# Kernel tuning notes

Measured on AMD Instinct MI355X. Metric: run time of the kernel, lower is better.

The kernel has to match this reference:

```python
import jax, jax.numpy as jnp
import numpy as np

H = 300          # node_hidden_dim (GINE output dim)
D = 2 * H        # set2set in_channels = 600
STEPS = 2        # num_step_set2_set


def _lstm_cell(x, h, c, W_ih, W_hh, b_ih, b_hh):
    # PyTorch LSTM gate order: i, f, g, o
    gates = x @ W_ih.T + h @ W_hh.T + b_ih + b_hh
    i, f, g, o = jnp.split(gates, 4, axis=-1)
    c = jax.nn.sigmoid(f) * c + jax.nn.sigmoid(i) * jnp.tanh(g)
    h = jax.nn.sigmoid(o) * jnp.tanh(c)
    return h, c


def _set2set(x, batch, num_graphs, W_ih, W_hh, b_ih, b_hh):
    # torch_geometric Set2Set with processing_steps=STEPS, 1-layer LSTM
    B = num_graphs
    q_star = jnp.zeros((B, 2 * D), x.dtype)
    h = jnp.zeros((B, D), x.dtype)
    c = jnp.zeros((B, D), x.dtype)
    for _ in range(STEPS):
        h, c = _lstm_cell(q_star, h, c, W_ih, W_hh, b_ih, b_hh)
        q = h                                   # [B, D]
        e = jnp.sum(x * q[batch], axis=-1)      # [N]
        emax = jax.ops.segment_max(e, batch, num_segments=B)
        a = jnp.exp(e - emax[batch])
        asum = jax.ops.segment_sum(a, batch, num_segments=B)
        a = a / (asum[batch] + 1e-16)           # segment softmax
        r = jax.ops.segment_sum(a[:, None] * x, batch, num_segments=B)
        q_star = jnp.concatenate([q, r], axis=-1)   # [B, 2D]
    return q_star


def _l2norm(x):
    return x / jnp.maximum(jnp.linalg.norm(x, axis=1, keepdims=True), 1e-12)


def setup_inputs() -> dict:
    key = jax.random.key(0)
    ks = jax.random.split(key, 8)
    Nu, Nv, B = 8192, 8192, 256
    solute_x = jax.random.normal(ks[0], (Nu, H), jnp.float32)
    solvent_x = jax.random.normal(ks[1], (Nv, H), jnp.float32)
    solute_batch = jnp.sort(jax.random.randint(ks[2], (Nu,), 0, B)).astype(jnp.int32)
    solvent_batch = jnp.sort(jax.random.randint(ks[3], (Nv,), 0, B)).astype(jnp.int32)
    lstm_W_ih = jax.random.normal(ks[4], (4 * D, 2 * D), jnp.float32) * 0.02
    lstm_W_hh = jax.random.normal(ks[5], (4 * D, D), jnp.float32) * 0.02
    lstm_b_ih = jnp.zeros((4 * D,), jnp.float32)
    lstm_b_hh = jnp.zeros((4 * D,), jnp.float32)
    pred_W = jax.random.normal(ks[6], (1, 8 * H), jnp.float32) * 0.02
    pred_b = jnp.zeros((1,), jnp.float32)
    return {
        "solute_x": solute_x, "solvent_x": solvent_x,
        "solute_batch": solute_batch, "solvent_batch": solvent_batch,
        "num_graphs": B,
        "lstm_W_ih": lstm_W_ih, "lstm_W_hh": lstm_W_hh,
        "lstm_b_ih": lstm_b_ih, "lstm_b_hh": lstm_b_hh,
        "pred_W": pred_W, "pred_b": pred_b,
    }


def reference(solute_x, solvent_x, solute_batch, solvent_batch, num_graphs,
              lstm_W_ih, lstm_W_hh, lstm_b_ih, lstm_b_hh, pred_W, pred_b):
    # F.normalize(dim=1)
    su = _l2norm(solute_x)    # [Nu, H]
    sv = _l2norm(solvent_x)   # [Nv, H]
    # len_map = solute_len.T @ solvent_len == same-pair membership mask
    mask = (solute_batch[:, None] == solvent_batch[None, :]).astype(su.dtype)
    interaction_map = (su @ sv.T) * mask          # [Nu, Nv]
    ret_interaction_map = interaction_map
    solvent_prime = interaction_map.T @ su        # [Nv, H]
    solute_prime = interaction_map @ sv           # [Nu, H]
    su2 = jnp.concatenate([su, solute_prime], axis=1)    # [Nu, 2H]
    sv2 = jnp.concatenate([sv, solvent_prime], axis=1)   # [Nv, 2H]
    su_s2s = _set2set(su2, solute_batch, num_graphs, lstm_W_ih, lstm_W_hh, lstm_b_ih, lstm_b_hh)
    sv_s2s = _set2set(sv2, solvent_batch, num_graphs, lstm_W_ih, lstm_W_hh, lstm_b_ih, lstm_b_hh)
    final = jnp.concatenate([su_s2s, sv_s2s], axis=1)    # [B, 8H]
    predictions = final @ pred_W.T + pred_b              # [B, 1]
    return predictions, ret_interaction_map
```

## Files before the change

kernel.cpp:

```cpp
#include <hip/hip_runtime.h>
#include <math.h>

#define HDIM 300
#define DDIM 600
#define NGR  256

typedef float vf4 __attribute__((ext_vector_type(4)));
typedef float vf2 __attribute__((ext_vector_type(2)));

__device__ __forceinline__ float wred_sum(float v){
  #pragma unroll
  for(int o=32;o;o>>=1) v += __shfl_xor(v,o,64);
  return v;
}
__device__ __forceinline__ float wred_max(float v){
  #pragma unroll
  for(int o=32;o;o>>=1) v = fmaxf(v,__shfl_xor(v,o,64));
  return v;
}
__device__ __forceinline__ float sigm(float x){ return 1.f/(1.f+expf(-x)); }

__device__ __forceinline__ void fill_row(int i, const int* __restrict__ ub,
    const int* __restrict__ voff, float* __restrict__ mapbase, int Nv, int tid){
  int g = ub[i];
  int js = voff[g], je = voff[g+1];
  float* mrow = mapbase + (size_t)i*Nv;
  const vf4 z4 = {0.f,0.f,0.f,0.f};
  int nf4 = Nv >> 2;
  for (int q4=tid; q4<nf4; q4+=256){
    int j0 = q4*4;
    if (j0+4 <= js || j0 >= je){
      __builtin_nontemporal_store(z4, (vf4*)(mrow + j0));
    } else {
      #pragma unroll
      for(int u=0;u<4;u++){ int j=j0+u; if (j<js || j>=je) mrow[j]=0.f; }
    }
  }
}

__global__ __launch_bounds__(256) void k_norm_off(const float* __restrict__ xu,
    const float* __restrict__ xv, float* __restrict__ su, float* __restrict__ sv,
    int Nu, int Nv, const int* __restrict__ ub, const int* __restrict__ vb,
    int* __restrict__ uoff, int* __restrict__ voff,
    const float* __restrict__ b_ih, const float* __restrict__ b_hh,
    float* __restrict__ h1, float* __restrict__ c1,
    const float* __restrict__ pb, float* __restrict__ outp,
    const float* __restrict__ Wih, const float* __restrict__ Whh,
    float* __restrict__ gbase){
  int NBn = (Nu + Nv) >> 2;
  int b = blockIdx.x;
  int tid = threadIdx.x, lane = tid & 63, w = tid >> 6;
  if (b == NBn){
    int t = tid;
    if (t < NGR){
      int lo=0, hi=Nu;
      while(lo<hi){ int m=(lo+hi)>>1; if (ub[m] < t) lo=m+1; else hi=m; }
      uoff[t]=lo;
      lo=0; hi=Nv;
      while(lo<hi){ int m=(lo+hi)>>1; if (vb[m] < t) lo=m+1; else hi=m; }
      voff[t]=lo;
      if (t==0){ uoff[NGR]=Nu; voff[NGR]=Nv; }
      outp[t] = pb[0];
    }
    for (int d=tid; d<DDIM; d+=256){
      float gi = b_ih[d]      + b_hh[d];
      float gg = b_ih[1200+d] + b_hh[1200+d];
      float go = b_ih[1800+d] + b_hh[1800+d];
      float c  = sigm(gi)*tanhf(gg);
      c1[d]=c; h1[d]=sigm(go)*tanhf(c);
    }
    return;
  }
  if (b > NBn){
    __shared__ float h1l[DDIM];
    for (int d=tid; d<DDIM; d+=256){
      float gi = b_ih[d]      + b_hh[d];
      float gg = b_ih[1200+d] + b_hh[1200+d];
      float go = b_ih[1800+d] + b_hh[1800+d];
      float c  = sigm(gi)*tanhf(gg);
      h1l[d]   = sigm(go)*tanhf(c);
    }
    __syncthreads();
    int n = (b - NBn - 1)*4 + w;
    const float* wi = Wih + (size_t)n*1200;
    const float* wh = Whh + (size_t)n*600;
    float s = 0.f;
    for (int k=lane; k<DDIM; k+=64) s += h1l[k]*(wi[k] + wh[k]);
    s = wred_sum(s);
    if (lane==0) gbase[n] = s + b_ih[n] + b_hh[n];
    return;
  }
  int wid = b*4 + w;
  const float* src; float* dst;
  if (wid < Nu){ src = xu + (size_t)wid*HDIM; dst = su + (size_t)wid*HDIM; }
  else         { src = xv + (size_t)(wid-Nu)*HDIM; dst = sv + (size_t)(wid-Nu)*HDIM; }
  const vf4* s4 = (const vf4*)src;
  vf4 A = s4[lane];
  vf4 Bv = (lane<11)? s4[64+lane] : (vf4){0.f,0.f,0.f,0.f};
  float s = A.x*A.x+A.y*A.y+A.z*A.z+A.w*A.w + Bv.x*Bv.x+Bv.y*Bv.y+Bv.z*Bv.z+Bv.w*Bv.w;
  s = wred_sum(s);
  float inv = 1.f / fmaxf(sqrtf(s), 1e-12f);
  vf4* d4 = (vf4*)dst;
  d4[lane] = A*inv;
  if (lane<11) d4[64+lane] = Bv*inv;
}

__global__ __launch_bounds__(256) void k_prime(const float* __restrict__ su,
    const float* __restrict__ sv, const int* __restrict__ ub,
    const int* __restrict__ vb, const int* __restrict__ uoff,
    const int* __restrict__ voff, float* __restrict__ spr,
    float* __restrict__ svp, float* __restrict__ e1u, float* __restrict__ e1v,
    const float* __restrict__ h1, float* __restrict__ mapbase, int Nu, int Nv){
  int b = blockIdx.x;
  int tid = threadIdx.x, lane = tid & 63, w = tid >> 6;
  int r = b % 3;
  if (r == 2){ fill_row(b/3, ub, voff, mapbase, Nv, tid); return; }
  int idx = (b/3)*2 + r;
  bool isU = (idx < Nu);
  int i = isU ? idx : idx - Nu;
  const float* xa = isU ? su : sv;
  const float* xb = isU ? sv : su;
  const int* mybatch = isU ? ub : vb;
  const int* ooff    = isU ? voff : uoff;
  float* prime = isU ? spr : svp;
  float* eout  = isU ? e1u : e1v;

  __shared__ __align__(16) float xrow[304];
  __shared__ __align__(16) float prl[4*304];
  __shared__ float qv[2*HDIM];
  __shared__ float red[4];
  const float* rowp = xa + (size_t)i*HDIM;
  for (int t=tid; t<HDIM;   t+=256) xrow[t] = rowp[t];
  for (int t=tid; t<2*HDIM; t+=256) qv[t]   = h1[t];
  int g = mybatch[i];
  int js = ooff[g], je = ooff[g+1];
  __syncthreads();

  const vf4* x4 = (const vf4*)xrow;
  vf4 xA = x4[lane];
  vf4 xB = (lane<11)? x4[64+lane] : (vf4){0.f,0.f,0.f,0.f};
  vf4 prA = {0.f,0.f,0.f,0.f}, prB = {0.f,0.f,0.f,0.f};
  for (int j = js + w; j < je; j += 4){
    const vf4* orow = (const vf4*)(xb + (size_t)j*HDIM);
    vf4 oA = orow[lane];
    vf4 oB = (lane<11)? orow[64+lane] : (vf4){0.f,0.f,0.f,0.f};
    float d = oA.x*xA.x + oA.y*xA.y + oA.z*xA.z + oA.w*xA.w
            + oB.x*xB.x + oB.y*xB.y + oB.z*xB.z + oB.w*xB.w;
    d = wred_sum(d);
    if (isU && lane==0) mapbase[(size_t)i*Nv + j] = d;
    prA += d * oA;
    prB += d * oB;
  }
  vf4* p4 = (vf4*)(prl + w*304);
  p4[lane] = prA;
  if (lane<11) p4[64+lane] = prB;
  __syncthreads();
  float ep = 0.f;
  for (int t=tid; t<HDIM; t+=256){
    float s = prl[t] + prl[304+t] + prl[608+t] + prl[912+t];
    prime[(size_t)i*HDIM + t] = s;
    ep += xrow[t]*qv[t] + s*qv[HDIM+t];
  }
  ep = wred_sum(ep);
  if (lane==0) red[w] = ep;
  __syncthreads();
  if (tid==0) eout[i] = red[0]+red[1]+red[2]+red[3];
}

__global__ __launch_bounds__(256) void k_r1(const float* __restrict__ su,
    const float* __restrict__ sv, const float* __restrict__ spr,
    const float* __restrict__ svp, const float* __restrict__ e1u,
    const float* __restrict__ e1v, const int* __restrict__ uoff,
    const int* __restrict__ voff, float* __restrict__ r1){
  int tid = threadIdx.x, lane = tid & 63, w = tid >> 6;
  int bs = blockIdx.x; int set = bs >> 8; int g = bs & 255;
  const float* x  = set? sv  : su;
  const float* pr = set? svp : spr;
  const float* e  = set? e1v : e1u;
  const int* off  = set? voff: uoff;
  __shared__ float al[2048]; __shared__ float red[4]; __shared__ float shv;
  int ns = off[g], ne = off[g+1]; int n = ne - ns;
  float m = -INFINITY;
  for (int t=ns+tid; t<ne; t+=256) m = fmaxf(m, e[t]);
  m = wred_max(m);
  if (lane==0) red[w]=m;
  __syncthreads();
  if (tid==0) shv = fmaxf(fmaxf(red[0],red[1]),fmaxf(red[2],red[3]));
  __syncthreads();
  float emax = shv;
  float s = 0.f;
  for (int t=tid; t<n; t+=256){ float a = expf(e[ns+t]-emax); if (t<2048) al[t]=a; s += a; }
  s = wred_sum(s);
  __syncthreads();
  if (lane==0) red[w]=s;
  __syncthreads();
  if (tid==0) shv = red[0]+red[1]+red[2]+red[3];
  __syncthreads();
  float inv = 1.f/(shv + 1e-16f);
  float acc[3] = {0.f,0.f,0.f};
  #pragma unroll 4
  for (int nn=0; nn<n; nn++){
    float a = (nn<2048)? al[nn] : expf(e[ns+nn]-emax);
    const float* xr = x  + (size_t)(ns+nn)*HDIM;
    const float* pp = pr + (size_t)(ns+nn)*HDIM;
    #pragma unroll
    for(int u=0;u<3;u++){ int c = tid + u*256; if (c<DDIM){
        float xv = (c<HDIM)? xr[c] : pp[c-HDIM]; acc[u] += a*xv; } }
  }
  #pragma unroll
  for(int u=0;u<3;u++){ int c = tid + u*256; if (c<DDIM) r1[(size_t)bs*DDIM + c] = acc[u]*inv; }
}

__global__ __launch_bounds__(256) void k_gemm_lstm(const float* __restrict__ r1,
    const float* __restrict__ Wih, const float* __restrict__ gbase,
    const float* __restrict__ c1, float* __restrict__ h2){
  __shared__ __align__(16) float smem[32*68];
  float* Al = smem;
  float* Bl = smem + 16*36;
  int tid = threadIdx.x;
  int d0  = blockIdx.x*16;
  int gs0 = blockIdx.y*32;
  int tx = tid & 15, ty = tid >> 4;
  float acc[2][4] = {};
  for (int kt=0; kt<600; kt+=16){
    int k = kt + tx;
    bool kok = (k < 600);
    #pragma unroll
    for (int u=0; u<2; u++){
      int rl = ty + u*16;
      Al[tx*36 + rl] = kok ? r1[(size_t)(gs0+rl)*DDIM + k] : 0.f;
    }
    #pragma unroll
    for (int u=0; u<4; u++){
      int cl = ty + u*16;
      int gate = cl >> 4, dd = cl & 15;
      int d = d0 + dd;
      Bl[tx*68 + cl] = (kok && d < 600)
          ? Wih[(size_t)(gate*600 + d)*1200 + 600 + k] : 0.f;
    }
    __syncthreads();
    #pragma unroll
    for (int kk=0; kk<16; kk++){
      vf2 av = ((const vf2*)(Al + kk*36))[ty];
      vf4 bv = ((const vf4*)(Bl + kk*68))[tx];
      float a[2]={av.x,av.y}, bb[4]={bv.x,bv.y,bv.z,bv.w};
      #pragma unroll
      for(int mm=0;mm<2;mm++)
        #pragma unroll
        for(int nn=0;nn<4;nn++) acc[mm][nn] += a[mm]*bb[nn];
    }
    __syncthreads();
  }
  #pragma unroll
  for (int mm=0; mm<2; mm++){
    vf4 o = {acc[mm][0], acc[mm][1], acc[mm][2], acc[mm][3]};
    ((vf4*)(smem + (ty*2+mm)*68))[tx] = o;
  }
  __syncthreads();
  int d_l = tid & 15, r0 = tid >> 4;
  int d = d0 + d_l;
  if (d < 600){
    float gb_i = gbase[d], gb_f = gbase[600+d], gb_g = gbase[1200+d], gb_o = gbase[1800+d];
    float cc1 = c1[d];
    #pragma unroll
    for (int u=0; u<2; u++){
      int rl = r0 + u*16;
      const float* gr = smem + rl*68;
      float gi = gr[d_l]      + gb_i;
      float gf = gr[16+d_l]   + gb_f;
      float gG = gr[32+d_l]   + gb_g;
      float go = gr[48+d_l]   + gb_o;
      float c  = sigm(gf)*cc1 + sigm(gi)*tanhf(gG);
      h2[(size_t)(gs0+rl)*DDIM + d] = sigm(go)*tanhf(c);
    }
  }
}

__global__ __launch_bounds__(256) void k_r2(const float* __restrict__ su,
    const float* __restrict__ sv, const float* __restrict__ spr,
    const float* __restrict__ svp, const int* __restrict__ uoff,
    const int* __restrict__ voff, const float* __restrict__ h2,
    const float* __restrict__ pW, float* __restrict__ e2u,
    float* __restrict__ e2v, float* __restrict__ outp){
  int tid = threadIdx.x, lane = tid & 63, w = tid >> 6;
  int bs = blockIdx.x; int set = bs >> 8; int g = bs & 255;
  const float* x  = set? sv  : su;
  const float* pr = set? svp : spr;
  const int* off  = set? voff: uoff;
  float* e2g      = set? e2v : e2u;
  __shared__ float q[DDIM]; __shared__ float e2l[128]; __shared__ float al[128];
  __shared__ float red[4]; __shared__ float shv;
  for (int t=tid; t<DDIM; t+=256) q[t] = h2[(size_t)bs*DDIM + t];
  int ns = off[g], ne = off[g+1]; int n = ne - ns;
  __syncthreads();
  #pragma unroll 2
  for (int node = ns + w; node < ne; node += 4){
    const float* xr = x  + (size_t)node*HDIM;
    const float* pp = pr + (size_t)node*HDIM;
    float d = 0.f;
    #pragma unroll
    for(int c=0;c<10;c++){ int k = lane + 64*c; if (k<DDIM){
        float xv = (k<HDIM)? xr[k] : pp[k-HDIM]; d += xv*q[k]; } }
    d = wred_sum(d);
    if (lane==0){ int t = node-ns; if (t<128) e2l[t] = d; else e2g[node] = d; }
  }
  __syncthreads();
  float m = -INFINITY;
  for (int t=tid; t<n; t+=256) m = fmaxf(m, (t<128)? e2l[t] : e2g[ns+t]);
  m = wred_max(m);
  if (lane==0) red[w]=m;
  __syncthreads();
  if (tid==0) shv = fmaxf(fmaxf(red[0],red[1]),fmaxf(red[2],red[3]));
  __syncthreads();
  float emax = shv;
  float s = 0.f;
  for (int t=tid; t<n; t+=256){
    float a = expf(((t<128)? e2l[t] : e2g[ns+t]) - emax);
    if (t<128) al[t]=a; else e2g[ns+t]=a;
    s += a;
  }
  s = wred_sum(s);
  __syncthreads();
  if (lane==0) red[w]=s;
  __syncthreads();
  if (tid==0) shv = red[0]+red[1]+red[2]+red[3];
  __syncthreads();
  float inv = 1.f/(shv + 1e-16f);
  float acc[3] = {0.f,0.f,0.f};
  #pragma unroll 4
  for (int nn=0; nn<n; nn++){
    float a = (nn<128)? al[nn] : e2g[ns+nn];
    const float* xr = x  + (size_t)(ns+nn)*HDIM;
    const float* pp = pr + (size_t)(ns+nn)*HDIM;
    #pragma unroll
    for(int u=0;u<3;u++){ int c = tid + u*256; if (c<DDIM){
        float xv = (c<HDIM)? xr[c] : pp[c-HDIM]; acc[u] += a*xv; } }
  }
  int hoff = set? 1200 : 0;
  float p = 0.f;
  #pragma unroll
  for(int u=0;u<3;u++){ int c = tid + u*256; if (c<DDIM) p += (acc[u]*inv)*pW[hoff+600+c]; }
  for (int t=tid; t<DDIM; t+=256) p += q[t]*pW[hoff+t];
  p = wred_sum(p);
  __syncthreads();
  if (lane==0) red[w] = p;
  __syncthreads();
  if (tid==0) atomicAdd(&outp[g], red[0]+red[1]+red[2]+red[3]);
}

extern "C" void kernel_launch(void* const* d_in, const int* in_sizes, int n_in,
                              void* d_out, int out_size, void* d_ws, size_t ws_size,
                              hipStream_t stream) {
  const float* solute_x  = (const float*)d_in[0];
  const float* solvent_x = (const float*)d_in[1];
  const int*   ub        = (const int*)d_in[2];
  const int*   vb        = (const int*)d_in[3];
  const float* Wih  = (const float*)d_in[5];
  const float* Whh  = (const float*)d_in[6];
  const float* b_ih = (const float*)d_in[7];
  const float* b_hh = (const float*)d_in[8];
  const float* pW   = (const float*)d_in[9];
  const float* pb   = (const float*)d_in[10];

  int Nu = in_sizes[0] / HDIM;
  int Nv = in_sizes[1] / HDIM;

  float* out = (float*)d_out;
  int predn = out_size - Nu*Nv;
  float* mapbase = out + predn;

  float* ws = (float*)d_ws;
  float* su    = ws;
  float* sv    = su    + (size_t)Nu*HDIM;
  float* spr   = sv    + (size_t)Nv*HDIM;
  float* svp   = spr   + (size_t)Nu*HDIM;
  float* e1u   = svp   + (size_t)Nv*HDIM;
  float* e1v   = e1u   + Nu;
  float* h1    = e1v   + Nv;
  float* c1    = h1    + DDIM;
  float* r1    = c1    + DDIM;
  float* gbase = r1    + 512*DDIM;
  float* h2    = gbase + 2400;
  int*   uoff  = (int*)(h2 + 512*DDIM);
  int*   voff  = uoff + 257;

  k_norm_off<<<dim3((Nu+Nv)/4 + 1 + 600), dim3(256), 0, stream>>>(
      solute_x, solvent_x, su, sv, Nu, Nv, ub, vb, uoff, voff,
      b_ih, b_hh, h1, c1, pb, out, Wih, Whh, gbase);
  k_prime<<<dim3(24576), dim3(256), 0, stream>>>(
      su, sv, ub, vb, uoff, voff, spr, svp, e1u, e1v, h1, mapbase, Nu, Nv);
  k_r1<<<dim3(512), dim3(256), 0, stream>>>(
      su, sv, spr, svp, e1u, e1v, uoff, voff, r1);
  k_gemm_lstm<<<dim3(38, 16), dim3(256), 0, stream>>>(r1, Wih, gbase, c1, h2);
  k_r2<<<dim3(512), dim3(256), 0, stream>>>(
      su, sv, spr, svp, uoff, voff, h2, pW, e1u, e1v, out);
}
```

Before: 520.9 us.

## Precompute per-row query dots in norm kernel and merge map zero-fill into prime kernel

The norm kernel now computes each normalized row's dot products with the two halves of the first-step query h1 and stores them per row. The prime kernel then forms the step-1 attention score algebraically as its own query dot plus the sum over neighbours of d times the partner's precomputed dot. This removes the per-block xrow/qv shared staging, a barrier and a separate reduction pass. The interaction-map zero-fill moves from dedicated blocks into the solute blocks, cutting the grid from three blocks per pair to one per row, at the cost of heavier solute blocks and extra workspace arrays.

```diff
diff --git a/kernel.cpp b/kernel.cpp
--- a/kernel.cpp
+++ b/kernel.cpp
@@ -19,24 +19,6 @@
   return v;
 }
 __device__ __forceinline__ float sigm(float x){ return 1.f/(1.f+expf(-x)); }
-
-__device__ __forceinline__ void fill_row(int i, const int* __restrict__ ub,
-    const int* __restrict__ voff, float* __restrict__ mapbase, int Nv, int tid){
-  int g = ub[i];
-  int js = voff[g], je = voff[g+1];
-  float* mrow = mapbase + (size_t)i*Nv;
-  const vf4 z4 = {0.f,0.f,0.f,0.f};
-  int nf4 = Nv >> 2;
-  for (int q4=tid; q4<nf4; q4+=256){
-    int j0 = q4*4;
-    if (j0+4 <= js || j0 >= je){
-      __builtin_nontemporal_store(z4, (vf4*)(mrow + j0));
-    } else {
-      #pragma unroll
-      for(int u=0;u<4;u++){ int j=j0+u; if (j<js || j>=je) mrow[j]=0.f; }
-    }
-  }
-}
 
 __global__ __launch_bounds__(256) void k_norm_off(const float* __restrict__ xu,
     const float* __restrict__ xv, float* __restrict__ su, float* __restrict__ sv,
@@ -46,10 +28,13 @@
     float* __restrict__ h1, float* __restrict__ c1,
     const float* __restrict__ pb, float* __restrict__ outp,
     const float* __restrict__ Wih, const float* __restrict__ Whh,
-    float* __restrict__ gbase){
+    float* __restrict__ gbase,
+    float* __restrict__ au, float* __restrict__ av,
+    float* __restrict__ tu, float* __restrict__ tv){
   int NBn = (Nu + Nv) >> 2;
   int b = blockIdx.x;
   int tid = threadIdx.x, lane = tid & 63, w = tid >> 6;
+  __shared__ __align__(16) float h1l[DDIM];
   if (b == NBn){
     int t = tid;
     if (t < NGR){
@@ -71,16 +56,15 @@
     }
     return;
   }
+  for (int d=tid; d<DDIM; d+=256){
+    float gi = b_ih[d]      + b_hh[d];
+    float gg = b_ih[1200+d] + b_hh[1200+d];
+    float go = b_ih[1800+d] + b_hh[1800+d];
+    float c  = sigm(gi)*tanhf(gg);
+    h1l[d]   = sigm(go)*tanhf(c);
+  }
+  __syncthreads();
   if (b > NBn){
-    __shared__ float h1l[DDIM];
-    for (int d=tid; d<DDIM; d+=256){
-      float gi = b_ih[d]      + b_hh[d];
-      float gg = b_ih[1200+d] + b_hh[1200+d];
-      float go = b_ih[1800+d] + b_hh[1800+d];
-      float c  = sigm(gi)*tanhf(gg);
-      h1l[d]   = sigm(go)*tanhf(c);
-    }
-    __syncthreads();
     int n = (b - NBn - 1)*4 + w;
     const float* wi = Wih + (size_t)n*1200;
     const float* wh = Whh + (size_t)n*600;
@@ -91,55 +75,68 @@
     return;
   }
   int wid = b*4 + w;
-  const float* src; float* dst;
-  if (wid < Nu){ src = xu + (size_t)wid*HDIM; dst = su + (size_t)wid*HDIM; }
-  else         { src = xv + (size_t)(wid-Nu)*HDIM; dst = sv + (size_t)(wid-Nu)*HDIM; }
+  const float* src; float* dst; float* aout; float* tout; int li;
+  if (wid < Nu){ li = wid; src = xu + (size_t)li*HDIM; dst = su + (size_t)li*HDIM;
+                 aout = au; tout = tu; }
+  else         { li = wid - Nu; src = xv + (size_t)li*HDIM; dst = sv + (size_t)li*HDIM;
+                 aout = av; tout = tv; }
   const vf4* s4 = (const vf4*)src;
   vf4 A = s4[lane];
   vf4 Bv = (lane<11)? s4[64+lane] : (vf4){0.f,0.f,0.f,0.f};
   float s = A.x*A.x+A.y*A.y+A.z*A.z+A.w*A.w + Bv.x*Bv.x+Bv.y*Bv.y+Bv.z*Bv.z+Bv.w*Bv.w;
   s = wred_sum(s);
   float inv = 1.f / fmaxf(sqrtf(s), 1e-12f);
+  vf4 A2 = A*inv, B2 = Bv*inv;
   vf4* d4 = (vf4*)dst;
-  d4[lane] = A*inv;
-  if (lane<11) d4[64+lane] = Bv*inv;
-}
-
-__global__ __launch_bounds__(256) void k_prime(const float* __restrict__ su,
+  d4[lane] = A2;
+  if (lane<11) d4[64+lane] = B2;
+  const vf4* q14 = (const vf4*)h1l;
+  const vf4* q24 = (const vf4*)(h1l + HDIM);
+  vf4 q1A = q14[lane];
+  vf4 q1B = (lane<11)? q14[64+lane] : (vf4){0.f,0.f,0.f,0.f};
+  vf4 q2A = q24[lane];
+  vf4 q2B = (lane<11)? q24[64+lane] : (vf4){0.f,0.f,0.f,0.f};
+  float aa = A2.x*q1A.x+A2.y*q1A.y+A2.z*q1A.z+A2.w*q1A.w
+           + B2.x*q1B.x+B2.y*q1B.y+B2.z*q1B.z+B2.w*q1B.w;
+  float tt = A2.x*q2A.x+A2.y*q2A.y+A2.z*q2A.z+A2.w*q2A.w
+           + B2.x*q2B.x+B2.y*q2B.y+B2.z*q2B.z+B2.w*q2B.w;
+  aa = wred_sum(aa);
+  tt = wred_sum(tt);
+  if (lane==0){ aout[li] = aa; tout[li] = tt; }
+}
+
+__global__ __launch_bounds__(256) void k_prime3(const float* __restrict__ su,
     const float* __restrict__ sv, const int* __restrict__ ub,
     const int* __restrict__ vb, const int* __restrict__ uoff,
     const int* __restrict__ voff, float* __restrict__ spr,
     float* __restrict__ svp, float* __restrict__ e1u, float* __restrict__ e1v,
-    const float* __restrict__ h1, float* __restrict__ mapbase, int Nu, int Nv){
+    const float* __restrict__ au, const float* __restrict__ av,
+    const float* __restrict__ tu, const float* __restrict__ tv,
+    float* __restrict__ mapbase, int Nu, int Nv){
   int b = blockIdx.x;
   int tid = threadIdx.x, lane = tid & 63, w = tid >> 6;
-  int r = b % 3;
-  if (r == 2){ fill_row(b/3, ub, voff, mapbase, Nv, tid); return; }
-  int idx = (b/3)*2 + r;
-  bool isU = (idx < Nu);
-  int i = isU ? idx : idx - Nu;
+  bool isU = (b < Nu);
+  int i = isU ? b : b - Nu;
   const float* xa = isU ? su : sv;
   const float* xb = isU ? sv : su;
   const int* mybatch = isU ? ub : vb;
   const int* ooff    = isU ? voff : uoff;
   float* prime = isU ? spr : svp;
   float* eout  = isU ? e1u : e1v;
-
-  __shared__ __align__(16) float xrow[304];
+  const float* aarr = isU ? au : av;
+  const float* tpar = isU ? tv : tu;
+
   __shared__ __align__(16) float prl[4*304];
-  __shared__ float qv[2*HDIM];
   __shared__ float red[4];
-  const float* rowp = xa + (size_t)i*HDIM;
-  for (int t=tid; t<HDIM;   t+=256) xrow[t] = rowp[t];
-  for (int t=tid; t<2*HDIM; t+=256) qv[t]   = h1[t];
+
   int g = mybatch[i];
   int js = ooff[g], je = ooff[g+1];
-  __syncthreads();
-
-  const vf4* x4 = (const vf4*)xrow;
-  vf4 xA = x4[lane];
-  vf4 xB = (lane<11)? x4[64+lane] : (vf4){0.f,0.f,0.f,0.f};
+  const vf4* xr4 = (const vf4*)(xa + (size_t)i*HDIM);
+  vf4 xA = xr4[lane];
+  vf4 xB = (lane<11)? xr4[64+lane] : (vf4){0.f,0.f,0.f,0.f};
+
   vf4 prA = {0.f,0.f,0.f,0.f}, prB = {0.f,0.f,0.f,0.f};
+  float ep = 0.f;
   for (int j = js + w; j < je; j += 4){
     const vf4* orow = (const vf4*)(xb + (size_t)j*HDIM);
     vf4 oA = orow[lane];
@@ -148,23 +145,34 @@
             + oB.x*xB.x + oB.y*xB.y + oB.z*xB.z + oB.w*xB.w;
     d = wred_sum(d);
     if (isU && lane==0) mapbase[(size_t)i*Nv + j] = d;
+    ep += d * tpar[j];
     prA += d * oA;
     prB += d * oB;
   }
   vf4* p4 = (vf4*)(prl + w*304);
   p4[lane] = prA;
   if (lane<11) p4[64+lane] = prB;
-  __syncthreads();
-  float ep = 0.f;
+  if (lane==0) red[w] = ep;
+  __syncthreads();
   for (int t=tid; t<HDIM; t+=256){
     float s = prl[t] + prl[304+t] + prl[608+t] + prl[912+t];
     prime[(size_t)i*HDIM + t] = s;
-    ep += xrow[t]*qv[t] + s*qv[HDIM+t];
-  }
-  ep = wred_sum(ep);
-  if (lane==0) red[w] = ep;
-  __syncthreads();
-  if (tid==0) eout[i] = red[0]+red[1]+red[2]+red[3];
+  }
+  if (tid==0) eout[i] = aarr[i] + red[0]+red[1]+red[2]+red[3];
+  if (isU){
+    float* mrow = mapbase + (size_t)i*Nv;
+    const vf4 z4 = {0.f,0.f,0.f,0.f};
+    int nf4 = Nv >> 2;
+    for (int q4=tid; q4<nf4; q4+=256){
+      int j0 = q4*4;
+      if (j0+4 <= js || j0 >= je){
+        __builtin_nontemporal_store(z4, (vf4*)(mrow + j0));
+      } else {
+        #pragma unroll
+        for(int u=0;u<4;u++){ int j=j0+u; if (j<js || j>=je) mrow[j]=0.f; }
+      }
+    }
+  }
 }
 
 __global__ __launch_bounds__(256) void k_r1(const float* __restrict__ su,
@@ -381,14 +389,19 @@
   float* r1    = c1    + DDIM;
   float* gbase = r1    + 512*DDIM;
   float* h2    = gbase + 2400;
-  int*   uoff  = (int*)(h2 + 512*DDIM);
+  float* au    = h2    + 512*DDIM;
+  float* av    = au    + Nu;
+  float* tu    = av    + Nv;
+  float* tv    = tu    + Nu;
+  int*   uoff  = (int*)(tv + Nv);
   int*   voff  = uoff + 257;
 
   k_norm_off<<<dim3((Nu+Nv)/4 + 1 + 600), dim3(256), 0, stream>>>(
       solute_x, solvent_x, su, sv, Nu, Nv, ub, vb, uoff, voff,
-      b_ih, b_hh, h1, c1, pb, out, Wih, Whh, gbase);
-  k_prime<<<dim3(24576), dim3(256), 0, stream>>>(
-      su, sv, ub, vb, uoff, voff, spr, svp, e1u, e1v, h1, mapbase, Nu, Nv);
+      b_ih, b_hh, h1, c1, pb, out, Wih, Whh, gbase, au, av, tu, tv);
+  k_prime3<<<dim3(Nu + Nv), dim3(256), 0, stream>>>(
+      su, sv, ub, vb, uoff, voff, spr, svp, e1u, e1v,
+      au, av, tu, tv, mapbase, Nu, Nv);
   k_r1<<<dim3(512), dim3(256), 0, stream>>>(
       su, sv, spr, svp, e1u, e1v, uoff, voff, r1);
   k_gemm_lstm<<<dim3(38, 16), dim3(256), 0, stream>>>(r1, Wih, gbase, c1, h2);
```

Result: slower. 533.5 us (+2.4%).
